# Kernel optimization log

Hardware: AMD Instinct MI355X
Metric: run time of the kernel (lower is better)

Reference implementation:

```python
import jax, jax.numpy as jnp
import numpy as np

B, V, CIN, H, W = 2, 4, 256, 96, 96
COUT, VS = 32, 64


def setup_inputs() -> dict:
    key = jax.random.key(0)
    k1, k2, k3, k4, k5 = jax.random.split(key, 5)
    features = jax.random.normal(k1, (B, V, CIN, H, W), dtype=jnp.float32)
    proj_matricies = jax.random.normal(k2, (B, V, 3, 4), dtype=jnp.float32)
    coord_volumes = jax.random.normal(k3, (B, VS, VS, VS, 3), dtype=jnp.float32) * 1000.0
    W_proc = jax.random.normal(k4, (COUT, CIN), dtype=jnp.float32) * 0.05
    b_proc = jax.random.normal(k5, (COUT,), dtype=jnp.float32) * 0.01
    return {"features": features, "proj_matricies": proj_matricies,
            "coord_volumes": coord_volumes, "W_proc": W_proc, "b_proc": b_proc}


def _bilinear_sample(feat, x, y):
    # feat: [C, H, W]; x, y: [N] pixel coords (align_corners=True mapping already applied)
    Hh, Ww = feat.shape[1], feat.shape[2]
    x0 = jnp.floor(x).astype(jnp.int32); x1 = x0 + 1
    y0 = jnp.floor(y).astype(jnp.int32); y1 = y0 + 1
    wx1 = x - x0; wx0 = 1.0 - wx1
    wy1 = y - y0; wy0 = 1.0 - wy1

    def gather(xi, yi):
        valid = ((xi >= 0) & (xi < Ww) & (yi >= 0) & (yi < Hh)).astype(feat.dtype)
        xc = jnp.clip(xi, 0, Ww - 1); yc = jnp.clip(yi, 0, Hh - 1)
        return feat[:, yc, xc] * valid  # [C, N] (zeros padding)

    return (gather(x0, y0) * (wx0 * wy0)
            + gather(x1, y0) * (wx1 * wy0)
            + gather(x0, y1) * (wx0 * wy1)
            + gather(x1, y1) * (wx1 * wy1))


def reference(features, proj_matricies, coord_volumes, W_proc, b_proc):
    b, v, cin, h, w = features.shape
    vs = coord_volumes.shape[1]
    # 1x1 conv (process_feature)
    feats = jnp.einsum('bvchw,oc->bvohw', features, W_proc) + b_proc[None, None, :, None, None]
    c = feats.shape[2]
    # homogeneous 3D grid points: [B, N, 4]
    pts = coord_volumes.reshape(b, -1, 3)
    pts_h = jnp.concatenate([pts, jnp.ones(pts.shape[:-1] + (1,), pts.dtype)], axis=-1)
    # project to image plane: [B, V, N, 3] homogeneous (u, v, w)
    proj_pts = jnp.einsum('bvij,bnj->bvni', proj_matricies, pts_h)
    wz = proj_pts[..., 2]
    invalid = wz <= 0.0
    wz_safe = jnp.where(wz == 0.0, 1.0, wz)
    u = proj_pts[..., 0] / wz_safe
    ve = proj_pts[..., 1] / wz_safe
    # normalized grid coords (faithful to original: x divided by feature_shape[0]=H, y by feature_shape[1]=W)
    gx = 2.0 * (u / h - 0.5)
    gy = 2.0 * (ve / w - 0.5)
    # align_corners=True pixel coords: x indexes width, y indexes height
    px = (gx + 1.0) * 0.5 * (w - 1)
    py = (gy + 1.0) * 0.5 * (h - 1)
    # sample per (batch, view): [B, V, C, N]
    sampled = jax.vmap(jax.vmap(_bilinear_sample))(feats, px, py)
    sampled = jnp.where(invalid[:, :, None, :], 0.0, sampled)
    # softmax over views per (b, c, voxel), weighted sum
    weights = jax.nn.softmax(sampled, axis=1)
    vol = jnp.sum(sampled * weights, axis=1)  # [B, C, N]
    return vol.reshape(b, c, vs, vs, vs)
```

## Files before the change

### kernel.cpp

```cpp
#include <hip/hip_runtime.h>
#include <hip/hip_bf16.h>

#define CIN   256
#define COUT  32
#define IMG_H 96
#define IMG_W 96
#define HW    (IMG_H*IMG_W)
#define NB    2
#define NV    4
#define VSZ   64
#define NVOX  (VSZ*VSZ*VSZ)

typedef __attribute__((ext_vector_type(2))) float f32x2;

__device__ __forceinline__ float fast_exp2(float x) {
    float r;
    asm("v_exp_f32 %0, %1" : "=v"(r) : "v"(x));
    return r;
}

__global__ __launch_bounds__(256) void conv1x1_kernel(
    const float* __restrict__ features,
    const float* __restrict__ Wp,
    const float* __restrict__ bp,
    __hip_bfloat16* __restrict__ out)
{
    const int og   = __builtin_amdgcn_readfirstlane((threadIdx.x >> 6) & 3);
    const int lane = threadIdx.x & 63;
    const int bv   = blockIdx.y;
    const int px   = blockIdx.x*64 + lane;
    const float* f     = features + (size_t)bv*CIN*HW + px;
    const float* wbase = Wp + (size_t)og*8*CIN;

    float acc[8];
    #pragma unroll
    for (int j = 0; j < 8; ++j) acc[j] = bp[og*8 + j];

    for (int cc = 0; cc < CIN; cc += 8) {
        float x[8];
        #pragma unroll
        for (int i = 0; i < 8; ++i)
            x[i] = f[(size_t)(cc + i)*HW];
        #pragma unroll
        for (int i = 0; i < 8; ++i) {
            #pragma unroll
            for (int j = 0; j < 8; ++j)
                acc[j] += x[i] * wbase[(size_t)j*CIN + cc + i];
        }
    }

    union { uint4 u4; __hip_bfloat16 h[8]; } pk;
    #pragma unroll
    for (int j = 0; j < 8; ++j) pk.h[j] = __float2bfloat16(acc[j]);
    *(uint4*)(out + ((size_t)(bv*HW + px))*COUT + og*8) = pk.u4;
}

__global__ __launch_bounds__(256, 4) void volgen_kernel(
    const __hip_bfloat16* __restrict__ feats,
    const float* __restrict__ proj,
    const float* __restrict__ coords,
    float* __restrict__ out)
{
    const int tid = threadIdx.x;
    const int b   = blockIdx.y;
    const int n   = blockIdx.x*256 + tid;

    const float* cp = coords + ((size_t)b*NVOX + n)*3;
    const float X = cp[0], Y = cp[1], Z = cp[2];

    const float LOG2E = 1.4426950408889634f;

    int   off[NV][4];
    float wgt[NV][4];
    #pragma unroll
    for (int v = 0; v < NV; ++v) {
        const float* P = proj + (size_t)(b*NV + v)*12;
        const float wz = P[8]*X + P[9]*Y + P[10]*Z + P[11];
        const bool  vz = wz > 0.f;
        const float rz = __builtin_amdgcn_rcpf(wz);
        float px = (P[0]*X + P[1]*Y + P[2]*Z + P[3]) * rz * (95.f/96.f);
        float py = (P[4]*X + P[5]*Y + P[6]*Z + P[7]) * rz * (95.f/96.f);
        px = vz ? px : 0.f;  py = vz ? py : 0.f;
        px = fminf(fmaxf(px, -1.0e6f), 1.0e6f);
        py = fminf(fmaxf(py, -1.0e6f), 1.0e6f);
        const float fx0 = floorf(px), fy0 = floorf(py);
        const int x0 = (int)fx0, y0 = (int)fy0, x1 = x0+1, y1 = y0+1;
        const float wx1 = px - fx0, wx0 = 1.f - wx1;
        const float wy1 = py - fy0, wy0 = 1.f - wy1;
        const bool vx0 = (unsigned)x0 < (unsigned)IMG_W;
        const bool vx1 = (unsigned)x1 < (unsigned)IMG_W;
        const bool vy0 = (unsigned)y0 < (unsigned)IMG_H;
        const bool vy1 = (unsigned)y1 < (unsigned)IMG_H;
        const int cx0 = min(max(x0, 0), IMG_W-1), cx1 = min(max(x1, 0), IMG_W-1);
        const int cy0 = min(max(y0, 0), IMG_H-1), cy1 = min(max(y1, 0), IMG_H-1);
        const int base = ((b*NV + v)*HW)*COUT*2;
        off[v][0] = base + (cy0*IMG_W + cx0)*(COUT*2);  wgt[v][0] = (vz & vx0 & vy0) ? wx0*wy0*LOG2E : 0.f;
        off[v][1] = base + (cy0*IMG_W + cx1)*(COUT*2);  wgt[v][1] = (vz & vx1 & vy0) ? wx1*wy0*LOG2E : 0.f;
        off[v][2] = base + (cy1*IMG_W + cx0)*(COUT*2);  wgt[v][2] = (vz & vx0 & vy1) ? wx0*wy1*LOG2E : 0.f;
        off[v][3] = base + (cy1*IMG_W + cx1)*(COUT*2);  wgt[v][3] = (vz & vx1 & vy1) ? wx1*wy1*LOG2E : 0.f;
    }

    const char* fb = (const char*)feats;
    const size_t ob = (size_t)b*COUT*NVOX + n;
    const float LN2 = 0.6931471805599453f;

    for (int ch0 = 0; ch0 < COUT; ch0 += 8) {
        f32x2 A2[4], B2[4];
        uint4 t[4], tn[4];

        #pragma unroll
        for (int c = 0; c < 4; ++c)
            t[c] = *(const uint4*)(fb + off[0][c] + ch0*2);

        #pragma unroll
        for (int v = 0; v < NV; ++v) {
            if (v < NV-1) {
                #pragma unroll
                for (int c = 0; c < 4; ++c)
                    tn[c] = *(const uint4*)(fb + off[v+1][c] + ch0*2);
            }

            f32x2 s2[4];
            #pragma unroll
            for (int c = 0; c < 4; ++c) {
                const float w = wgt[v][c];
                const f32x2 w2 = { w, w };
                const unsigned tu[4] = { t[c].x, t[c].y, t[c].z, t[c].w };
                #pragma unroll
                for (int k = 0; k < 4; ++k) {
                    f32x2 f2;
                    f2.x = __uint_as_float(tu[k] << 16);
                    f2.y = __uint_as_float(tu[k] & 0xffff0000u);
                    if (c == 0) s2[k] = w2 * f2;
                    else        s2[k] += w2 * f2;
                }
            }

            #pragma unroll
            for (int k = 0; k < 4; ++k) {
                f32x2 e2;
                e2.x = fast_exp2(s2[k].x);
                e2.y = fast_exp2(s2[k].y);
                if (v == 0) { A2[k] = e2;  B2[k] = s2[k]*e2; }
                else        { A2[k] += e2; B2[k] += s2[k]*e2; }
            }

            if (v < NV-1) {
                #pragma unroll
                for (int c = 0; c < 4; ++c) t[c] = tn[c];
            }
        }

        #pragma unroll
        for (int k = 0; k < 4; ++k) {
            out[ob + (size_t)(ch0 + 2*k    )*NVOX] = B2[k].x * __builtin_amdgcn_rcpf(A2[k].x) * LN2;
            out[ob + (size_t)(ch0 + 2*k + 1)*NVOX] = B2[k].y * __builtin_amdgcn_rcpf(A2[k].y) * LN2;
        }
    }
}

extern "C" void kernel_launch(void* const* d_in, const int* in_sizes, int n_in,
                              void* d_out, int out_size, void* d_ws, size_t ws_size,
                              hipStream_t stream)
{
    const float* features = (const float*)d_in[0];
    const float* proj     = (const float*)d_in[1];
    const float* coords   = (const float*)d_in[2];
    const float* Wp       = (const float*)d_in[3];
    const float* bp       = (const float*)d_in[4];
    float* out = (float*)d_out;
    __hip_bfloat16* featsT = (__hip_bfloat16*)d_ws;

    hipLaunchKernelGGL(conv1x1_kernel, dim3(HW/64, NB*NV), dim3(256), 0, stream,
                       features, Wp, bp, featsT);
    hipLaunchKernelGGL(volgen_kernel, dim3(NVOX/256, NB), dim3(256), 0, stream,
                       featsT, proj, coords, out);
}
```

Baseline: 179.0 us.

## Stage conv1x1 input tiles in LDS with double-buffered global_load_lds

The 1x1 conv previously had each of the 4 waves in a block load the same 64-pixel feature column from global memory, so every input was read four times. Now each wave loads a quarter of a 64-channel tile straight into LDS with global_load_lds, and all waves read the tile from LDS. The next tile is prefetched into a second buffer while the current one is computed. This cuts redundant global traffic and overlaps loads with FMAs, but adds 32 KB of LDS per block and a barrier per tile, which may reduce occupancy.

After: 252.7 us. 41.2% more time.

```diff
diff --git a/kernel.cpp b/kernel.cpp
--- a/kernel.cpp
+++ b/kernel.cpp
@@ -10,6 +10,7 @@
 #define NV    4
 #define VSZ   64
 #define NVOX  (VSZ*VSZ*VSZ)
+#define CH_TILE 64
 
 typedef __attribute__((ext_vector_type(2))) float f32x2;
 
@@ -19,40 +20,59 @@
     return r;
 }
 
+__device__ __forceinline__ void gload_lds4(const float* g, float* l) {
+    __builtin_amdgcn_global_load_lds(
+        (const __attribute__((address_space(1))) void*)g,
+        (__attribute__((address_space(3))) void*)l,
+        4, 0, 0);
+}
+
 __global__ __launch_bounds__(256) void conv1x1_kernel(
     const float* __restrict__ features,
     const float* __restrict__ Wp,
     const float* __restrict__ bp,
     __hip_bfloat16* __restrict__ out)
 {
+    __shared__ float sbuf[2][CH_TILE*64];
     const int og   = __builtin_amdgcn_readfirstlane((threadIdx.x >> 6) & 3);
     const int lane = threadIdx.x & 63;
     const int bv   = blockIdx.y;
-    const int px   = blockIdx.x*64 + lane;
-    const float* f     = features + (size_t)bv*CIN*HW + px;
+    const int px0  = blockIdx.x*64;
+    const float* fpx   = features + (size_t)bv*CIN*HW + px0 + lane;
     const float* wbase = Wp + (size_t)og*8*CIN;
 
     float acc[8];
     #pragma unroll
     for (int j = 0; j < 8; ++j) acc[j] = bp[og*8 + j];
 
-    for (int cc = 0; cc < CIN; cc += 8) {
-        float x[8];
+    #pragma unroll
+    for (int i = 0; i < 16; ++i)
+        gload_lds4(fpx + (size_t)(og*16 + i)*HW, &sbuf[0][(og*16 + i)*64]);
+    __syncthreads();
+
+    #pragma unroll
+    for (int t = 0; t < CIN/CH_TILE; ++t) {
+        const int cur = t & 1;
+        if (t + 1 < CIN/CH_TILE) {
+            #pragma unroll
+            for (int i = 0; i < 16; ++i)
+                gload_lds4(fpx + (size_t)((t+1)*CH_TILE + og*16 + i)*HW,
+                           &sbuf[cur ^ 1][(og*16 + i)*64]);
+        }
         #pragma unroll
-        for (int i = 0; i < 8; ++i)
-            x[i] = f[(size_t)(cc + i)*HW];
-        #pragma unroll
-        for (int i = 0; i < 8; ++i) {
+        for (int c = 0; c < CH_TILE; ++c) {
+            const float x = sbuf[cur][c*64 + lane];
             #pragma unroll
             for (int j = 0; j < 8; ++j)
-                acc[j] += x[i] * wbase[(size_t)j*CIN + cc + i];
+                acc[j] += x * wbase[(size_t)j*CIN + t*CH_TILE + c];
         }
+        __syncthreads();
     }
 
     union { uint4 u4; __hip_bfloat16 h[8]; } pk;
     #pragma unroll
     for (int j = 0; j < 8; ++j) pk.h[j] = __float2bfloat16(acc[j]);
-    *(uint4*)(out + ((size_t)(bv*HW + px))*COUT + og*8) = pk.u4;
+    *(uint4*)(out + ((size_t)(bv*HW + px0 + lane))*COUT + og*8) = pk.u4;
 }
 
 __global__ __launch_bounds__(256, 4) void volgen_kernel(
```

## Split conv input channels across waves with LDS reduction; pipeline volgen loads across chunks

Applied to the files above, without the earlier changes.

The 1x1 conv kernel now has each wave handle 64 input channels for all 32 outputs, instead of all 256 inputs for 8 outputs. Partial sums are combined through shared memory, so each feature element is loaded once per block rather than four times. The cost is more registers for the 32 accumulators plus an LDS round trip and a barrier. Separately, the volgen loop over channel chunks is fully unrolled and prefetches the next chunk's first-view texels during the last view, so load latency overlaps across chunk boundaries.

New measurement: 222.9 us. 24.5% more time.

```diff
diff --git a/kernel.cpp b/kernel.cpp
--- a/kernel.cpp
+++ b/kernel.cpp
@@ -25,34 +25,51 @@
     const float* __restrict__ bp,
     __hip_bfloat16* __restrict__ out)
 {
+    __shared__ float red[4][COUT][64];
     const int og   = __builtin_amdgcn_readfirstlane((threadIdx.x >> 6) & 3);
     const int lane = threadIdx.x & 63;
     const int bv   = blockIdx.y;
-    const int px   = blockIdx.x*64 + lane;
-    const float* f     = features + (size_t)bv*CIN*HW + px;
-    const float* wbase = Wp + (size_t)og*8*CIN;
+    const int px0  = blockIdx.x*64;
+    const float* f = features + (size_t)bv*CIN*HW + (size_t)og*64*HW + px0 + lane;
 
-    float acc[8];
+    float acc[COUT];
     #pragma unroll
-    for (int j = 0; j < 8; ++j) acc[j] = bp[og*8 + j];
+    for (int j = 0; j < COUT; ++j) acc[j] = 0.f;
 
-    for (int cc = 0; cc < CIN; cc += 8) {
-        float x[8];
+    #pragma unroll
+    for (int h = 0; h < 2; ++h) {
+        float x[32];
         #pragma unroll
-        for (int i = 0; i < 8; ++i)
-            x[i] = f[(size_t)(cc + i)*HW];
+        for (int i = 0; i < 32; ++i)
+            x[i] = f[(size_t)(h*32 + i)*HW];
         #pragma unroll
-        for (int i = 0; i < 8; ++i) {
+        for (int j = 0; j < COUT; ++j) {
+            const float* wrow = Wp + (size_t)j*CIN + og*64 + h*32;
+            float a0 = 0.f, a1 = 0.f, a2 = 0.f, a3 = 0.f;
             #pragma unroll
-            for (int j = 0; j < 8; ++j)
-                acc[j] += x[i] * wbase[(size_t)j*CIN + cc + i];
+            for (int i = 0; i < 32; i += 4) {
+                a0 += x[i  ]*wrow[i  ];
+                a1 += x[i+1]*wrow[i+1];
+                a2 += x[i+2]*wrow[i+2];
+                a3 += x[i+3]*wrow[i+3];
+            }
+            acc[j] += (a0 + a1) + (a2 + a3);
         }
     }
 
-    union { uint4 u4; __hip_bfloat16 h[8]; } pk;
     #pragma unroll
-    for (int j = 0; j < 8; ++j) pk.h[j] = __float2bfloat16(acc[j]);
-    *(uint4*)(out + ((size_t)(bv*HW + px))*COUT + og*8) = pk.u4;
+    for (int j = 0; j < COUT; ++j)
+        red[og][j][lane] = acc[j];
+    __syncthreads();
+
+    union { uint4 u4; __hip_bfloat16 hh[8]; } pk;
+    #pragma unroll
+    for (int j = 0; j < 8; ++j) {
+        const int ch = og*8 + j;
+        pk.hh[j] = __float2bfloat16(red[0][ch][lane] + red[1][ch][lane]
+                                  + red[2][ch][lane] + red[3][ch][lane] + bp[ch]);
+    }
+    *(uint4*)(out + ((size_t)(bv*HW + px0 + lane))*COUT + og*8) = pk.u4;
 }
 
 __global__ __launch_bounds__(256, 4) void volgen_kernel(
@@ -104,20 +121,24 @@
     const size_t ob = (size_t)b*COUT*NVOX + n;
     const float LN2 = 0.6931471805599453f;
 
+    uint4 t[4], tn[4];
+    #pragma unroll
+    for (int c = 0; c < 4; ++c)
+        t[c] = *(const uint4*)(fb + off[0][c]);
+
+    #pragma unroll
     for (int ch0 = 0; ch0 < COUT; ch0 += 8) {
         f32x2 A2[4], B2[4];
-        uint4 t[4], tn[4];
-
-        #pragma unroll
-        for (int c = 0; c < 4; ++c)
-            t[c] = *(const uint4*)(fb + off[0][c] + ch0*2);
 
         #pragma unroll
         for (int v = 0; v < NV; ++v) {
-            if (v < NV-1) {
+            const bool last = (v == NV-1) && (ch0 + 8 >= COUT);
+            if (!last) {
+                const int nv  = (v < NV-1) ? v+1 : 0;
+                const int nc0 = (v < NV-1) ? ch0 : ch0+8;
                 #pragma unroll
                 for (int c = 0; c < 4; ++c)
-                    tn[c] = *(const uint4*)(fb + off[v+1][c] + ch0*2);
+                    tn[c] = *(const uint4*)(fb + off[nv][c] + nc0*2);
             }
 
             f32x2 s2[4];
@@ -145,7 +166,7 @@
                 else        { A2[k] += e2; B2[k] += s2[k]*e2; }
             }
 
-            if (v < NV-1) {
+            if (!last) {
                 #pragma unroll
                 for (int c = 0; c < 4; ++c) t[c] = tn[c];
             }
```

## Split conv K-dimension across waves and deepen volgen gather prefetch pipeline

Applied to the files above, without the earlier changes.

The 1x1 conv kernel now uses 512 threads per block. Two wave halves each reduce half of the input channels, and their partial sums are combined through shared memory before the bias is added and the result is written as bf16. This doubles the waves in flight for the memory-bound conv, at the cost of a barrier and LDS traffic. The volgen kernel flattens the channel-group and view loops into one 16-step fully unrolled loop with a two-deep prefetch of gathered feature texels, so loads overlap across channel-group boundaries. That raises register pressure under the existing launch bounds.

After: 208.4 us. 16.5% more time.

```diff
diff --git a/kernel.cpp b/kernel.cpp
--- a/kernel.cpp
+++ b/kernel.cpp
@@ -19,24 +19,27 @@
     return r;
 }
 
-__global__ __launch_bounds__(256) void conv1x1_kernel(
+__global__ __launch_bounds__(512) void conv1x1_kernel(
     const float* __restrict__ features,
     const float* __restrict__ Wp,
     const float* __restrict__ bp,
     __hip_bfloat16* __restrict__ out)
 {
-    const int og   = __builtin_amdgcn_readfirstlane((threadIdx.x >> 6) & 3);
+    __shared__ float red[COUT][2][64];
+    const int wid  = threadIdx.x >> 6;
+    const int og   = __builtin_amdgcn_readfirstlane(wid & 3);
+    const int kh   = __builtin_amdgcn_readfirstlane(wid >> 2);
     const int lane = threadIdx.x & 63;
     const int bv   = blockIdx.y;
     const int px   = blockIdx.x*64 + lane;
-    const float* f     = features + (size_t)bv*CIN*HW + px;
-    const float* wbase = Wp + (size_t)og*8*CIN;
+    const float* f     = features + (size_t)bv*CIN*HW + (size_t)kh*128*HW + px;
+    const float* wbase = Wp + (size_t)og*8*CIN + kh*128;
 
     float acc[8];
     #pragma unroll
-    for (int j = 0; j < 8; ++j) acc[j] = bp[og*8 + j];
+    for (int j = 0; j < 8; ++j) acc[j] = 0.f;
 
-    for (int cc = 0; cc < CIN; cc += 8) {
+    for (int cc = 0; cc < 128; cc += 8) {
         float x[8];
         #pragma unroll
         for (int i = 0; i < 8; ++i)
@@ -49,10 +52,20 @@
         }
     }
 
-    union { uint4 u4; __hip_bfloat16 h[8]; } pk;
     #pragma unroll
-    for (int j = 0; j < 8; ++j) pk.h[j] = __float2bfloat16(acc[j]);
-    *(uint4*)(out + ((size_t)(bv*HW + px))*COUT + og*8) = pk.u4;
+    for (int j = 0; j < 8; ++j)
+        red[og*8 + j][kh][lane] = acc[j];
+    __syncthreads();
+
+    if (kh == 0) {
+        union { uint4 u4; __hip_bfloat16 hh[8]; } pk;
+        #pragma unroll
+        for (int j = 0; j < 8; ++j) {
+            const int ch = og*8 + j;
+            pk.hh[j] = __float2bfloat16(red[ch][0][lane] + red[ch][1][lane] + bp[ch]);
+        }
+        *(uint4*)(out + ((size_t)(bv*HW + px))*COUT + og*8) = pk.u4;
+    }
 }
 
 __global__ __launch_bounds__(256, 4) void volgen_kernel(
@@ -104,58 +117,64 @@
     const size_t ob = (size_t)b*COUT*NVOX + n;
     const float LN2 = 0.6931471805599453f;
 
-    for (int ch0 = 0; ch0 < COUT; ch0 += 8) {
-        f32x2 A2[4], B2[4];
-        uint4 t[4], tn[4];
+    uint4 t[4], tn[4], tnn[4];
+    #pragma unroll
+    for (int c = 0; c < 4; ++c)
+        t[c] = *(const uint4*)(fb + off[0][c]);
+    #pragma unroll
+    for (int c = 0; c < 4; ++c)
+        tn[c] = *(const uint4*)(fb + off[1][c]);
 
+    f32x2 A2[4], B2[4];
+
+    #pragma unroll
+    for (int s = 0; s < 16; ++s) {
+        const int v   = s & 3;
+        const int ch0 = (s >> 2) * 8;
+
+        if (s + 2 < 16) {
+            const int v2  = (s+2) & 3;
+            const int c20 = ((s+2) >> 2) * 8;
+            #pragma unroll
+            for (int c = 0; c < 4; ++c)
+                tnn[c] = *(const uint4*)(fb + off[v2][c] + c20*2);
+        }
+
+        f32x2 s2[4];
         #pragma unroll
-        for (int c = 0; c < 4; ++c)
-            t[c] = *(const uint4*)(fb + off[0][c] + ch0*2);
-
-        #pragma unroll
-        for (int v = 0; v < NV; ++v) {
-            if (v < NV-1) {
-                #pragma unroll
-                for (int c = 0; c < 4; ++c)
-                    tn[c] = *(const uint4*)(fb + off[v+1][c] + ch0*2);
-            }
-
-            f32x2 s2[4];
-            #pragma unroll
-            for (int c = 0; c < 4; ++c) {
-                const float w = wgt[v][c];
-                const f32x2 w2 = { w, w };
-                const unsigned tu[4] = { t[c].x, t[c].y, t[c].z, t[c].w };
-                #pragma unroll
-                for (int k = 0; k < 4; ++k) {
-                    f32x2 f2;
-                    f2.x = __uint_as_float(tu[k] << 16);
-                    f2.y = __uint_as_float(tu[k] & 0xffff0000u);
-                    if (c == 0) s2[k] = w2 * f2;
-                    else        s2[k] += w2 * f2;
-                }
-            }
-
+        for (int c = 0; c < 4; ++c) {
+            const float w = wgt[v][c];
+            const f32x2 w2 = { w, w };
+            const unsigned tu[4] = { t[c].x, t[c].y, t[c].z, t[c].w };
             #pragma unroll
             for (int k = 0; k < 4; ++k) {
-                f32x2 e2;
-                e2.x = fast_exp2(s2[k].x);
-                e2.y = fast_exp2(s2[k].y);
-                if (v == 0) { A2[k] = e2;  B2[k] = s2[k]*e2; }
-                else        { A2[k] += e2; B2[k] += s2[k]*e2; }
-            }
-
-            if (v < NV-1) {
-                #pragma unroll
-                for (int c = 0; c < 4; ++c) t[c] = tn[c];
+                f32x2 f2;
+                f2.x = __uint_as_float(tu[k] << 16);
+                f2.y = __uint_as_float(tu[k] & 0xffff0000u);
+                if (c == 0) s2[k] = w2 * f2;
+                else        s2[k] += w2 * f2;
             }
         }
 
         #pragma unroll
         for (int k = 0; k < 4; ++k) {
-            out[ob + (size_t)(ch0 + 2*k    )*NVOX] = B2[k].x * __builtin_amdgcn_rcpf(A2[k].x) * LN2;
-            out[ob + (size_t)(ch0 + 2*k + 1)*NVOX] = B2[k].y * __builtin_amdgcn_rcpf(A2[k].y) * LN2;
+            f32x2 e2;
+            e2.x = fast_exp2(s2[k].x);
+            e2.y = fast_exp2(s2[k].y);
+            if (v == 0) { A2[k] = e2;  B2[k] = s2[k]*e2; }
+            else        { A2[k] += e2; B2[k] += s2[k]*e2; }
         }
+
+        if (v == 3) {
+            #pragma unroll
+            for (int k = 0; k < 4; ++k) {
+                out[ob + (size_t)(ch0 + 2*k    )*NVOX] = B2[k].x * __builtin_amdgcn_rcpf(A2[k].x) * LN2;
+                out[ob + (size_t)(ch0 + 2*k + 1)*NVOX] = B2[k].y * __builtin_amdgcn_rcpf(A2[k].y) * LN2;
+            }
+        }
+
+        #pragma unroll
+        for (int c = 0; c < 4; ++c) { t[c] = tn[c]; tn[c] = tnn[c]; }
     }
 }
 
@@ -171,7 +190,7 @@
     float* out = (float*)d_out;
     __hip_bfloat16* featsT = (__hip_bfloat16*)d_ws;
 
-    hipLaunchKernelGGL(conv1x1_kernel, dim3(HW/64, NB*NV), dim3(256), 0, stream,
+    hipLaunchKernelGGL(conv1x1_kernel, dim3(HW/64, NB*NV), dim3(512), 0, stream,
                        features, Wp, bp, featsT);
     hipLaunchKernelGGL(volgen_kernel, dim3(NVOX/256, NB), dim3(256), 0, stream,
                        featsT, proj, coords, out);
```
